# Kernel tuning notes

Measured on AMD Instinct MI355X. Metric: run time of the kernel, lower is better.

Reference implementation:

```python
import math
import jax, jax.numpy as jnp
import numpy as np

M = 0.4
H = 0.333
S = 64.0
T_ALPHA = 1.0
EPS = 1e-3
BM0 = 20.0   # initial batch_mean buffer
BS0 = 100.0  # initial batch_std buffer


def setup_inputs() -> dict:
    key = jax.random.key(0)
    k1, k2, k3 = jax.random.split(key, 3)
    N, C = 2048, 50000
    cosine = jax.random.uniform(k1, (N, C), dtype=jnp.float32)  # in [0,1) subset of valid cosine range
    norms = jax.random.uniform(k2, (N, 1), dtype=jnp.float32)
    label = jax.random.randint(k3, (N,), 0, C, dtype=jnp.int64)
    return {"cosine": cosine, "norms": norms, "label": label}


def reference(cosine, norms, label):
    N, C = cosine.shape
    valid = (label != -1)                      # rows that get a margin (partial-FC)
    validf = valid.astype(cosine.dtype)

    # norm statistics are detached in the original (clone().detach())
    safe_norms = jax.lax.stop_gradient(jnp.clip(norms, 1e-3, 100.0))
    mean = safe_norms.mean()
    std = jnp.std(safe_norms, ddof=1)          # torch .std() is unbiased
    batch_mean = mean * T_ALPHA + (1.0 - T_ALPHA) * BM0
    batch_std = std * T_ALPHA + (1.0 - T_ALPHA) * BS0

    margin_scaler = jnp.clip((safe_norms - batch_mean) / (batch_std + EPS) * H, -1.0, 1.0)[:, 0]  # [N]

    rows = jnp.arange(N)
    lab = jnp.where(valid, label, 0)

    # angular margin: add g_angular at the label column, then clip full positive rows
    theta = jnp.arccos(cosine)                 # [N, C]
    g_angular = -M * margin_scaler * validf    # [N]
    theta = theta.at[rows, lab].add(g_angular)
    theta = jnp.where(valid[:, None], jnp.clip(theta, EPS, math.pi - EPS), theta)
    cos_m = jnp.cos(theta)

    # additive margin at the label column
    g_add = (M + M * margin_scaler) * validf   # [N]
    cos_m = cos_m.at[rows, lab].add(-g_add)

    return cos_m * S
```

## Files before the change

kernel.cpp:

```cpp
#include <hip/hip_runtime.h>
#include <math.h>


#define MARGIN    0.4f
#define HPARAM    0.333f
#define SCALE     64.0f
#define EPSF      1e-3f
#define COS_EPS   0.999999500000041653f
#define PI_M_EPS  3.140592653589793f

typedef float f32x4 __attribute__((ext_vector_type(4)));

__global__ __launch_bounds__(256) void prep_kernel(const float* __restrict__ norms,
                                                   const int*   __restrict__ label,
                                                   const float* __restrict__ cosine,
                                                   int N, int C,
                                                   float* __restrict__ ws) {
    __shared__ double sdata[256];
    const int t = threadIdx.x;

    double s = 0.0;
    for (int i = t; i < N; i += 256) {
        float v = fminf(fmaxf(norms[i], 1e-3f), 100.0f);
        s += (double)v;
    }
    sdata[t] = s;
    __syncthreads();
    for (int k = 128; k > 0; k >>= 1) {
        if (t < k) sdata[t] += sdata[t + k];
        __syncthreads();
    }
    const double mean = sdata[0] / (double)N;
    __syncthreads();

    double sq = 0.0;
    for (int i = t; i < N; i += 256) {
        float v = fminf(fmaxf(norms[i], 1e-3f), 100.0f);
        double d = (double)v - mean;
        sq += d * d;
    }
    sdata[t] = sq;
    __syncthreads();
    for (int k = 128; k > 0; k >>= 1) {
        if (t < k) sdata[t] += sdata[t + k];
        __syncthreads();
    }
    const float bm = (float)mean;
    const float bs = (float)sqrt(sdata[0] / (double)(N - 1));
    if (t == 0) { ws[0] = bm; ws[1] = bs; }
    __syncthreads();

    for (int row = t; row < N; row += 256) {
        const int lab = label[row];
        float fix = 0.0f;
        if (lab != -1) {
            const float sn = fminf(fmaxf(norms[row], 1e-3f), 100.0f);
            const float ms = fminf(fmaxf((sn - bm) / (bs + EPSF) * HPARAM, -1.0f), 1.0f);
            const float xv = cosine[(size_t)row * (size_t)C + (size_t)lab];
            float theta = acosf(xv) - MARGIN * ms;
            theta = fminf(fmaxf(theta, EPSF), PI_M_EPS);
            fix = (cosf(theta) - (MARGIN + MARGIN * ms)) * SCALE;
        }
        ws[2 + row] = fix;
    }
}

__global__ __launch_bounds__(256) void adaface_main(
        const float* __restrict__ cosine,
        const int*   __restrict__ label,
        const float* __restrict__ ws,
        float*       __restrict__ out,
        int C4) {
    const int row = blockIdx.x;
    const int lab = label[row];
    const bool valid = (lab != -1);
    const int lab4 = lab >> 2;
    const int labk = lab & 3;
    const float fix = ws[2 + row];

    const f32x4* __restrict__ src = reinterpret_cast<const f32x4*>(cosine) + (size_t)row * (size_t)C4;
    f32x4*       __restrict__ dst = reinterpret_cast<f32x4*>(out)          + (size_t)row * (size_t)C4;

    if (valid) {
        for (int c4 = threadIdx.x; c4 < C4; c4 += 256) {
            f32x4 x = __builtin_nontemporal_load(src + c4);
            f32x4 y;
            y.x = fminf(fmaxf(x.x, -COS_EPS), COS_EPS) * SCALE;
            y.y = fminf(fmaxf(x.y, -COS_EPS), COS_EPS) * SCALE;
            y.z = fminf(fmaxf(x.z, -COS_EPS), COS_EPS) * SCALE;
            y.w = fminf(fmaxf(x.w, -COS_EPS), COS_EPS) * SCALE;
            if (c4 == lab4) {
                y.x = (labk == 0) ? fix : y.x;
                y.y = (labk == 1) ? fix : y.y;
                y.z = (labk == 2) ? fix : y.z;
                y.w = (labk == 3) ? fix : y.w;
            }
            __builtin_nontemporal_store(y, dst + c4);
        }
    } else {
        for (int c4 = threadIdx.x; c4 < C4; c4 += 256) {
            f32x4 x = __builtin_nontemporal_load(src + c4);
            f32x4 y = { x.x * SCALE, x.y * SCALE, x.z * SCALE, x.w * SCALE };
            __builtin_nontemporal_store(y, dst + c4);
        }
    }
}

extern "C" void kernel_launch(void* const* d_in, const int* in_sizes, int n_in,
                              void* d_out, int out_size, void* d_ws, size_t ws_size,
                              hipStream_t stream) {
    const float* cosine = (const float*)d_in[0];
    const float* norms  = (const float*)d_in[1];
    const int*   label  = (const int*)d_in[2];
    float*       out    = (float*)d_out;
    float*       ws     = (float*)d_ws;

    const int N  = in_sizes[2];
    const int C  = in_sizes[0] / N;
    const int C4 = C / 4;

    prep_kernel<<<1, 256, 0, stream>>>(norms, label, cosine, N, C, ws);
    adaface_main<<<N, 256, 0, stream>>>(cosine, label, ws, out, C4);
}
```

Baseline: 185.9 us.

## Fuse norm statistics into main kernel, drop nontemporal ops, unroll by two

Removes the separate single-block prep kernel. Each row block now recomputes the batch mean and std of the norms itself, and the thread that owns the label column computes the margin-corrected value. This drops a serialized launch and the workspace round trip. In exchange, every block redundantly reduces all N norms in double precision with barriers. The streaming loop is also unrolled by two and switched from nontemporal to ordinary loads and stores.

```diff
diff --git a/kernel.cpp b/kernel.cpp
--- a/kernel.cpp
+++ b/kernel.cpp
@@ -11,49 +11,59 @@
 
 typedef float f32x4 __attribute__((ext_vector_type(4)));
 
-__global__ __launch_bounds__(256) void prep_kernel(const float* __restrict__ norms,
-                                                   const int*   __restrict__ label,
-                                                   const float* __restrict__ cosine,
-                                                   int N, int C,
-                                                   float* __restrict__ ws) {
-    __shared__ double sdata[256];
-    const int t = threadIdx.x;
+__device__ __forceinline__ f32x4 clipscale(f32x4 x) {
+    f32x4 y;
+    y.x = fminf(fmaxf(x.x, -COS_EPS), COS_EPS) * SCALE;
+    y.y = fminf(fmaxf(x.y, -COS_EPS), COS_EPS) * SCALE;
+    y.z = fminf(fmaxf(x.z, -COS_EPS), COS_EPS) * SCALE;
+    y.w = fminf(fmaxf(x.w, -COS_EPS), COS_EPS) * SCALE;
+    return y;
+}
 
-    double s = 0.0;
-    for (int i = t; i < N; i += 256) {
-        float v = fminf(fmaxf(norms[i], 1e-3f), 100.0f);
-        s += (double)v;
-    }
-    sdata[t] = s;
-    __syncthreads();
-    for (int k = 128; k > 0; k >>= 1) {
-        if (t < k) sdata[t] += sdata[t + k];
+__global__ __launch_bounds__(256) void adaface_fused(
+        const float* __restrict__ cosine,
+        const float* __restrict__ norms,
+        const int*   __restrict__ label,
+        float*       __restrict__ out,
+        int N, int C, int C4) {
+    const int t   = threadIdx.x;
+    const int row = blockIdx.x;
+    const int lab = label[row];
+
+    const f32x4* __restrict__ src = reinterpret_cast<const f32x4*>(cosine) + (size_t)row * (size_t)C4;
+    f32x4*       __restrict__ dst = reinterpret_cast<f32x4*>(out)          + (size_t)row * (size_t)C4;
+
+    if (lab != -1) {
+        __shared__ double sdata[256];
+        double s = 0.0;
+        for (int i = t; i < N; i += 256)
+            s += (double)fminf(fmaxf(norms[i], 1e-3f), 100.0f);
+        sdata[t] = s;
         __syncthreads();
-    }
-    const double mean = sdata[0] / (double)N;
-    __syncthreads();
+        for (int k = 128; k > 0; k >>= 1) {
+            if (t < k) sdata[t] += sdata[t + k];
+            __syncthreads();
+        }
+        const double mean = sdata[0] / (double)N;
+        __syncthreads();
+        double sq = 0.0;
+        for (int i = t; i < N; i += 256) {
+            double d = (double)fminf(fmaxf(norms[i], 1e-3f), 100.0f) - mean;
+            sq += d * d;
+        }
+        sdata[t] = sq;
+        __syncthreads();
+        for (int k = 128; k > 0; k >>= 1) {
+            if (t < k) sdata[t] += sdata[t + k];
+            __syncthreads();
+        }
+        const float bm = (float)mean;
+        const float bs = (float)sqrt(sdata[0] / (double)(N - 1));
 
-    double sq = 0.0;
-    for (int i = t; i < N; i += 256) {
-        float v = fminf(fmaxf(norms[i], 1e-3f), 100.0f);
-        double d = (double)v - mean;
-        sq += d * d;
-    }
-    sdata[t] = sq;
-    __syncthreads();
-    for (int k = 128; k > 0; k >>= 1) {
-        if (t < k) sdata[t] += sdata[t + k];
-        __syncthreads();
-    }
-    const float bm = (float)mean;
-    const float bs = (float)sqrt(sdata[0] / (double)(N - 1));
-    if (t == 0) { ws[0] = bm; ws[1] = bs; }
-    __syncthreads();
-
-    for (int row = t; row < N; row += 256) {
-        const int lab = label[row];
+        const int lab4 = lab >> 2;
+        const int labk = lab & 3;
         float fix = 0.0f;
-        if (lab != -1) {
+        if (t == (lab4 & 255)) {
             const float sn = fminf(fmaxf(norms[row], 1e-3f), 100.0f);
             const float ms = fminf(fmaxf((sn - bm) / (bs + EPSF) * HPARAM, -1.0f), 1.0f);
             const float xv = cosine[(size_t)row * (size_t)C + (size_t)lab];
@@ -61,47 +71,52 @@
             theta = fminf(fmaxf(theta, EPSF), PI_M_EPS);
             fix = (cosf(theta) - (MARGIN + MARGIN * ms)) * SCALE;
         }
-        ws[2 + row] = fix;
-    }
-}
 
-__global__ __launch_bounds__(256) void adaface_main(
-        const float* __restrict__ cosine,
-        const int*   __restrict__ label,
-        const float* __restrict__ ws,
-        float*       __restrict__ out,
-        int C4) {
-    const int row = blockIdx.x;
-    const int lab = label[row];
-    const bool valid = (lab != -1);
-    const int lab4 = lab >> 2;
-    const int labk = lab & 3;
-    const float fix = ws[2 + row];
-
-    const f32x4* __restrict__ src = reinterpret_cast<const f32x4*>(cosine) + (size_t)row * (size_t)C4;
-    f32x4*       __restrict__ dst = reinterpret_cast<f32x4*>(out)          + (size_t)row * (size_t)C4;
-
-    if (valid) {
-        for (int c4 = threadIdx.x; c4 < C4; c4 += 256) {
-            f32x4 x = __builtin_nontemporal_load(src + c4);
-            f32x4 y;
-            y.x = fminf(fmaxf(x.x, -COS_EPS), COS_EPS) * SCALE;
-            y.y = fminf(fmaxf(x.y, -COS_EPS), COS_EPS) * SCALE;
-            y.z = fminf(fmaxf(x.z, -COS_EPS), COS_EPS) * SCALE;
-            y.w = fminf(fmaxf(x.w, -COS_EPS), COS_EPS) * SCALE;
+        int c4 = t;
+        for (; c4 + 256 < C4; c4 += 512) {
+            f32x4 x0 = src[c4];
+            f32x4 x1 = src[c4 + 256];
+            f32x4 y0 = clipscale(x0);
+            f32x4 y1 = clipscale(x1);
+            if (c4 == lab4) {
+                y0.x = (labk == 0) ? fix : y0.x;
+                y0.y = (labk == 1) ? fix : y0.y;
+                y0.z = (labk == 2) ? fix : y0.z;
+                y0.w = (labk == 3) ? fix : y0.w;
+            }
+            if (c4 + 256 == lab4) {
+                y1.x = (labk == 0) ? fix : y1.x;
+                y1.y = (labk == 1) ? fix : y1.y;
+                y1.z = (labk == 2) ? fix : y1.z;
+                y1.w = (labk == 3) ? fix : y1.w;
+            }
+            dst[c4]       = y0;
+            dst[c4 + 256] = y1;
+        }
+        for (; c4 < C4; c4 += 256) {
+            f32x4 y = clipscale(src[c4]);
             if (c4 == lab4) {
                 y.x = (labk == 0) ? fix : y.x;
                 y.y = (labk == 1) ? fix : y.y;
                 y.z = (labk == 2) ? fix : y.z;
                 y.w = (labk == 3) ? fix : y.w;
             }
-            __builtin_nontemporal_store(y, dst + c4);
+            dst[c4] = y;
         }
     } else {
-        for (int c4 = threadIdx.x; c4 < C4; c4 += 256) {
-            f32x4 x = __builtin_nontemporal_load(src + c4);
+        int c4 = t;
+        for (; c4 + 256 < C4; c4 += 512) {
+            f32x4 x0 = src[c4];
+            f32x4 x1 = src[c4 + 256];
+            f32x4 y0 = { x0.x * SCALE, x0.y * SCALE, x0.z * SCALE, x0.w * SCALE };
+            f32x4 y1 = { x1.x * SCALE, x1.y * SCALE, x1.z * SCALE, x1.w * SCALE };
+            dst[c4]       = y0;
+            dst[c4 + 256] = y1;
+        }
+        for (; c4 < C4; c4 += 256) {
+            f32x4 x = src[c4];
             f32x4 y = { x.x * SCALE, x.y * SCALE, x.z * SCALE, x.w * SCALE };
-            __builtin_nontemporal_store(y, dst + c4);
+            dst[c4] = y;
         }
     }
 }
@@ -113,12 +128,10 @@
     const float* norms  = (const float*)d_in[1];
     const int*   label  = (const int*)d_in[2];
     float*       out    = (float*)d_out;
-    float*       ws     = (float*)d_ws;
 
     const int N  = in_sizes[2];
     const int C  = in_sizes[0] / N;
     const int C4 = C / 4;
 
-    prep_kernel<<<1, 256, 0, stream>>>(norms, label, cosine, N, C, ws);
-    adaface_main<<<N, 256, 0, stream>>>(cosine, label, ws, out, C4);
+    adaface_fused<<<N, 256, 0, stream>>>(cosine, norms, label, out, N, C, C4);
 }
```

Result: no change. 184.3 us (-0.9%).

## Split into flat clamp-copy pass followed by single-block label patch kernel

Applied to the files above, without the earlier changes.

The per-row main kernel is replaced by a flat grid-stride clamp-and-scale copy that issues four independent vector loads per thread, which should raise memory-level parallelism. A separate single 1024-thread kernel then computes the norm statistics and overwrites each label element in the output. The old prep kernel no longer has to finish before the bulk copy can start, and the per-element label comparison leaves the hot loop. In exchange, invalid rows are now clamped too, which differs from the reference only when a value sits very close to ±1. The two passes also depend on stream ordering.

```diff
diff --git a/kernel.cpp b/kernel.cpp
--- a/kernel.cpp
+++ b/kernel.cpp
@@ -11,22 +11,48 @@
 
 typedef float f32x4 __attribute__((ext_vector_type(4)));
 
-__global__ __launch_bounds__(256) void prep_kernel(const float* __restrict__ norms,
-                                                   const int*   __restrict__ label,
-                                                   const float* __restrict__ cosine,
-                                                   int N, int C,
-                                                   float* __restrict__ ws) {
-    __shared__ double sdata[256];
+__device__ __forceinline__ f32x4 clipscale(f32x4 x) {
+    f32x4 y;
+    y.x = fminf(fmaxf(x.x, -COS_EPS), COS_EPS) * SCALE;
+    y.y = fminf(fmaxf(x.y, -COS_EPS), COS_EPS) * SCALE;
+    y.z = fminf(fmaxf(x.z, -COS_EPS), COS_EPS) * SCALE;
+    y.w = fminf(fmaxf(x.w, -COS_EPS), COS_EPS) * SCALE;
+    return y;
+}
+
+__global__ __launch_bounds__(256) void clampcopy(const f32x4* __restrict__ src,
+                                                 f32x4* __restrict__ dst,
+                                                 long total4) {
+    const long S = (long)gridDim.x * 256L;
+    long i = (long)blockIdx.x * 256L + threadIdx.x;
+    for (; i + 3L * S < total4; i += 4L * S) {
+        f32x4 a = __builtin_nontemporal_load(src + i);
+        f32x4 b = __builtin_nontemporal_load(src + i + S);
+        f32x4 c = __builtin_nontemporal_load(src + i + 2L * S);
+        f32x4 d = __builtin_nontemporal_load(src + i + 3L * S);
+        __builtin_nontemporal_store(clipscale(a), dst + i);
+        __builtin_nontemporal_store(clipscale(b), dst + i + S);
+        __builtin_nontemporal_store(clipscale(c), dst + i + 2L * S);
+        __builtin_nontemporal_store(clipscale(d), dst + i + 3L * S);
+    }
+    for (; i < total4; i += S)
+        __builtin_nontemporal_store(clipscale(__builtin_nontemporal_load(src + i)), dst + i);
+}
+
+__global__ __launch_bounds__(1024) void patch_kernel(const float* __restrict__ norms,
+                                                     const int*   __restrict__ label,
+                                                     const float* __restrict__ cosine,
+                                                     float*       __restrict__ out,
+                                                     int N, int C) {
+    __shared__ double sdata[1024];
     const int t = threadIdx.x;
 
     double s = 0.0;
-    for (int i = t; i < N; i += 256) {
-        float v = fminf(fmaxf(norms[i], 1e-3f), 100.0f);
-        s += (double)v;
-    }
+    for (int i = t; i < N; i += 1024)
+        s += (double)fminf(fmaxf(norms[i], 1e-3f), 100.0f);
     sdata[t] = s;
     __syncthreads();
-    for (int k = 128; k > 0; k >>= 1) {
+    for (int k = 512; k > 0; k >>= 1) {
         if (t < k) sdata[t] += sdata[t + k];
         __syncthreads();
     }
@@ -34,74 +60,28 @@
     __syncthreads();
 
     double sq = 0.0;
-    for (int i = t; i < N; i += 256) {
-        float v = fminf(fmaxf(norms[i], 1e-3f), 100.0f);
-        double d = (double)v - mean;
+    for (int i = t; i < N; i += 1024) {
+        double d = (double)fminf(fmaxf(norms[i], 1e-3f), 100.0f) - mean;
         sq += d * d;
     }
     sdata[t] = sq;
     __syncthreads();
-    for (int k = 128; k > 0; k >>= 1) {
+    for (int k = 512; k > 0; k >>= 1) {
         if (t < k) sdata[t] += sdata[t + k];
         __syncthreads();
     }
     const float bm = (float)mean;
     const float bs = (float)sqrt(sdata[0] / (double)(N - 1));
-    if (t == 0) { ws[0] = bm; ws[1] = bs; }
-    __syncthreads();
 
-    for (int row = t; row < N; row += 256) {
+    for (int row = t; row < N; row += 1024) {
         const int lab = label[row];
-        float fix = 0.0f;
         if (lab != -1) {
             const float sn = fminf(fmaxf(norms[row], 1e-3f), 100.0f);
             const float ms = fminf(fmaxf((sn - bm) / (bs + EPSF) * HPARAM, -1.0f), 1.0f);
-            const float xv = cosine[(size_t)row * (size_t)C + (size_t)lab];
-            float theta = acosf(xv) - MARGIN * ms;
+            const size_t idx = (size_t)row * (size_t)C + (size_t)lab;
+            float theta = acosf(cosine[idx]) - MARGIN * ms;
             theta = fminf(fmaxf(theta, EPSF), PI_M_EPS);
-            fix = (cosf(theta) - (MARGIN + MARGIN * ms)) * SCALE;
-        }
-        ws[2 + row] = fix;
-    }
-}
-
-__global__ __launch_bounds__(256) void adaface_main(
-        const float* __restrict__ cosine,
-        const int*   __restrict__ label,
-        const float* __restrict__ ws,
-        float*       __restrict__ out,
-        int C4) {
-    const int row = blockIdx.x;
-    const int lab = label[row];
-    const bool valid = (lab != -1);
-    const int lab4 = lab >> 2;
-    const int labk = lab & 3;
-    const float fix = ws[2 + row];
-
-    const f32x4* __restrict__ src = reinterpret_cast<const f32x4*>(cosine) + (size_t)row * (size_t)C4;
-    f32x4*       __restrict__ dst = reinterpret_cast<f32x4*>(out)          + (size_t)row * (size_t)C4;
-
-    if (valid) {
-        for (int c4 = threadIdx.x; c4 < C4; c4 += 256) {
-            f32x4 x = __builtin_nontemporal_load(src + c4);
-            f32x4 y;
-            y.x = fminf(fmaxf(x.x, -COS_EPS), COS_EPS) * SCALE;
-            y.y = fminf(fmaxf(x.y, -COS_EPS), COS_EPS) * SCALE;
-            y.z = fminf(fmaxf(x.z, -COS_EPS), COS_EPS) * SCALE;
-            y.w = fminf(fmaxf(x.w, -COS_EPS), COS_EPS) * SCALE;
-            if (c4 == lab4) {
-                y.x = (labk == 0) ? fix : y.x;
-                y.y = (labk == 1) ? fix : y.y;
-                y.z = (labk == 2) ? fix : y.z;
-                y.w = (labk == 3) ? fix : y.w;
-            }
-            __builtin_nontemporal_store(y, dst + c4);
-        }
-    } else {
-        for (int c4 = threadIdx.x; c4 < C4; c4 += 256) {
-            f32x4 x = __builtin_nontemporal_load(src + c4);
-            f32x4 y = { x.x * SCALE, x.y * SCALE, x.z * SCALE, x.w * SCALE };
-            __builtin_nontemporal_store(y, dst + c4);
+            out[idx] = (cosf(theta) - (MARGIN + MARGIN * ms)) * SCALE;
         }
     }
 }
@@ -113,12 +93,12 @@
     const float* norms  = (const float*)d_in[1];
     const int*   label  = (const int*)d_in[2];
     float*       out    = (float*)d_out;
-    float*       ws     = (float*)d_ws;
 
-    const int N  = in_sizes[2];
-    const int C  = in_sizes[0] / N;
-    const int C4 = C / 4;
+    const int  N      = in_sizes[2];
+    const int  C      = in_sizes[0] / N;
+    const long total4 = (long)in_sizes[0] / 4;
 
-    prep_kernel<<<1, 256, 0, stream>>>(norms, label, cosine, N, C, ws);
-    adaface_main<<<N, 256, 0, stream>>>(cosine, label, ws, out, C4);
+    clampcopy<<<2048, 256, 0, stream>>>(reinterpret_cast<const f32x4*>(cosine),
+                                        reinterpret_cast<f32x4*>(out), total4);
+    patch_kernel<<<1, 1024, 0, stream>>>(norms, label, cosine, out, N, C);
 }
```

Measured after the change: 199.7 us. +7.4%, slower.
